# Performance work log

Measured on AMD Instinct MI355X. Metric: run time of the kernel, lower is better.

Reference implementation:

```python
import jax, jax.numpy as jnp
import numpy as np

N, E = 50000, 800000
IN, HID, H, OUT, NLAYERS = 128, 32, 4, 1, 3
F_HID = HID * H  # 128, width between layers


def _glorot(key, shape, scale=0.05):
    return jax.random.normal(key, shape, dtype=jnp.float32) * scale


def setup_inputs() -> dict:
    key = jax.random.key(0)
    ks = jax.random.split(key, 20)
    x = jax.random.normal(ks[0], (N, IN), dtype=jnp.float32)
    edge_index = jax.random.randint(ks[1], (2, E), 0, N, dtype=jnp.int64)
    # layer 0 params (in=IN)
    W_l0 = _glorot(ks[2], (IN, F_HID)); b_l0 = jnp.zeros((F_HID,), jnp.float32)
    W_r0 = _glorot(ks[3], (IN, F_HID)); b_r0 = jnp.zeros((F_HID,), jnp.float32)
    att0 = _glorot(ks[4], (H, HID));    bo0 = jnp.zeros((F_HID,), jnp.float32)
    # layers 1..NLAYERS-1 stacked (in=F_HID)
    L = NLAYERS - 1
    W_l = _glorot(ks[5], (L, F_HID, F_HID)); b_l = jnp.zeros((L, F_HID), jnp.float32)
    W_r = _glorot(ks[6], (L, F_HID, F_HID)); b_r = jnp.zeros((L, F_HID), jnp.float32)
    att = _glorot(ks[7], (L, H, HID));        bo = jnp.zeros((L, F_HID), jnp.float32)
    # final linear
    W_f = _glorot(ks[8], (F_HID, OUT)); b_f = jnp.zeros((OUT,), jnp.float32)
    return dict(x=x, edge_index=edge_index,
                W_l0=W_l0, b_l0=b_l0, W_r0=W_r0, b_r0=b_r0, att0=att0, bo0=bo0,
                W_l=W_l, b_l=b_l, W_r=W_r, b_r=b_r, att=att, bo=bo,
                W_f=W_f, b_f=b_f)


def gatv2_layer(x, src, dst, Wl, bl, Wr, br, a, bo):
    # x: [N, Fin] -> [N, H*HID]. PyG GATv2Conv, concat=True, slope=0.2.
    xl = (x @ Wl + bl).reshape(N, H, HID)  # source transform (messages)
    xr = (x @ Wr + br).reshape(N, H, HID)  # target transform
    z = jax.nn.leaky_relu(xl[src] + xr[dst], 0.2)        # [E', H, HID]
    logits = jnp.einsum('ehc,hc->eh', z, a)              # [E', H]
    m = jax.ops.segment_max(logits, dst, num_segments=N)
    m = jnp.where(jnp.isfinite(m), m, 0.0)
    ex = jnp.exp(logits - m[dst])
    denom = jax.ops.segment_sum(ex, dst, num_segments=N)
    alpha = ex / jnp.maximum(denom[dst], 1e-16)          # segment softmax per dst
    out = jax.ops.segment_sum(xl[src] * alpha[:, :, None], dst, num_segments=N)
    return out.reshape(N, F_HID) + bo


def reference(x, edge_index, W_l0, b_l0, W_r0, b_r0, att0, bo0,
              W_l, b_l, W_r, b_r, att, bo, W_f, b_f):
    loop = jnp.arange(N, dtype=edge_index.dtype)  # PyG default add_self_loops=True
    src = jnp.concatenate([edge_index[0], loop])
    dst = jnp.concatenate([edge_index[1], loop])
    # dropout is identity in eval mode
    h = jax.nn.elu(gatv2_layer(x, src, dst, W_l0, b_l0, W_r0, b_r0, att0, bo0))
    for i in range(NLAYERS - 1):
        h = jax.nn.elu(gatv2_layer(h, src, dst, W_l[i], b_l[i], W_r[i], b_r[i], att[i], bo[i]))
    return h @ W_f + b_f  # [N, OUT]
```

## Files before the change

kernel.cpp:

```cpp
#include <hip/hip_runtime.h>
#include <math.h>

#define N_NODES 50000
#define F 128
#define NEDGE 800000
#define NB_SCAN 49

static __device__ __forceinline__ int imin(int a, int b) { return a < b ? a : b; }

__global__ __launch_bounds__(256) void gemm128(
    const float* __restrict__ A,
    const float* __restrict__ Wl, const float* __restrict__ bl,
    const float* __restrict__ Wr, const float* __restrict__ br,
    float* __restrict__ xl, float* __restrict__ xr)
{
    const float* W = blockIdx.y ? Wr : Wl;
    const float* b = blockIdx.y ? br : bl;
    float*       O = blockIdx.y ? xr : xl;

    __shared__ float As[32][132];
    __shared__ float Ws[32][132];

    const int tid = threadIdx.x;
    const int tx = tid & 15, ty = tid >> 4;
    const int R0 = blockIdx.x * 128;

    float acc[8][8];
#pragma unroll
    for (int i = 0; i < 8; ++i)
#pragma unroll
        for (int j = 0; j < 8; ++j) acc[i][j] = 0.f;

    for (int kt = 0; kt < 4; ++kt) {
#pragma unroll
        for (int i = 0; i < 4; ++i) {
            int f = tid + i * 256;
            int row = f >> 3, kq = f & 7;
            int gr = R0 + row;
            float4 v = make_float4(0.f, 0.f, 0.f, 0.f);
            if (gr < N_NODES) v = *(const float4*)&A[(size_t)gr * F + kt * 32 + kq * 4];
            As[kq * 4 + 0][row] = v.x; As[kq * 4 + 1][row] = v.y;
            As[kq * 4 + 2][row] = v.z; As[kq * 4 + 3][row] = v.w;
        }
#pragma unroll
        for (int i = 0; i < 4; ++i) {
            int f = tid + i * 256;
            int k = f >> 5, cq = f & 31;
            *(float4*)&Ws[k][cq * 4] = *(const float4*)&W[(size_t)(kt * 32 + k) * F + cq * 4];
        }
        __syncthreads();
#pragma unroll
        for (int k = 0; k < 32; ++k) {
            float a[8], w[8];
            *(float4*)&a[0] = *(const float4*)&As[k][ty * 8];
            *(float4*)&a[4] = *(const float4*)&As[k][ty * 8 + 4];
            *(float4*)&w[0] = *(const float4*)&Ws[k][tx * 8];
            *(float4*)&w[4] = *(const float4*)&Ws[k][tx * 8 + 4];
#pragma unroll
            for (int i = 0; i < 8; ++i)
#pragma unroll
                for (int j = 0; j < 8; ++j) acc[i][j] += a[i] * w[j];
        }
        __syncthreads();
    }
#pragma unroll
    for (int i = 0; i < 8; ++i) {
        int gr = R0 + ty * 8 + i;
        if (gr < N_NODES) {
#pragma unroll
            for (int j = 0; j < 8; ++j) acc[i][j] += b[tx * 8 + j];
            *(float4*)&O[(size_t)gr * F + tx * 8]     = make_float4(acc[i][0], acc[i][1], acc[i][2], acc[i][3]);
            *(float4*)&O[(size_t)gr * F + tx * 8 + 4] = make_float4(acc[i][4], acc[i][5], acc[i][6], acc[i][7]);
        }
    }
}

__global__ void k_hist(const int* __restrict__ dst, int* __restrict__ deg)
{
    for (int i = blockIdx.x * blockDim.x + threadIdx.x; i < NEDGE;
         i += gridDim.x * blockDim.x)
        atomicAdd(&deg[dst[i]], 1);
}

__global__ __launch_bounds__(1024) void k_reduce(const int* __restrict__ deg, int* __restrict__ bsum)
{
    __shared__ int s[1024];
    int i = blockIdx.x * 1024 + threadIdx.x;
    s[threadIdx.x] = (i < N_NODES) ? deg[i] + 1 : 0;
    __syncthreads();
    for (int d = 512; d > 0; d >>= 1) {
        if (threadIdx.x < d) s[threadIdx.x] += s[threadIdx.x + d];
        __syncthreads();
    }
    if (threadIdx.x == 0) bsum[blockIdx.x] = s[0];
}

__global__ void k_scan_bsum(const int* __restrict__ bsum, int* __restrict__ boff, int nb)
{
    if (blockIdx.x == 0 && threadIdx.x == 0) {
        int run = 0;
        for (int bb = 0; bb < nb; ++bb) { boff[bb] = run; run += bsum[bb]; }
    }
}

__global__ __launch_bounds__(1024) void k_scan(const int* __restrict__ deg, const int* __restrict__ boff,
                                               int* __restrict__ off, int* __restrict__ cursor)
{
    __shared__ int s[1024];
    int i = blockIdx.x * 1024 + threadIdx.x;
    int v = (i < N_NODES) ? deg[i] + 1 : 0;
    s[threadIdx.x] = v;
    __syncthreads();
    for (int d = 1; d < 1024; d <<= 1) {
        int tv = (threadIdx.x >= d) ? s[threadIdx.x - d] : 0;
        __syncthreads();
        s[threadIdx.x] += tv;
        __syncthreads();
    }
    int excl = s[threadIdx.x] - v + boff[blockIdx.x];
    if (i < N_NODES) { off[i] = excl; cursor[i] = excl; }
    if (i == N_NODES - 1) off[N_NODES] = excl + v;
}

__global__ void k_scatter(const int* __restrict__ src, const int* __restrict__ dst,
                          int* __restrict__ cursor, int* __restrict__ adj)
{
    for (int i = blockIdx.x * blockDim.x + threadIdx.x; i < NEDGE;
         i += gridDim.x * blockDim.x) {
        int p = atomicAdd(&cursor[dst[i]], 1);
        adj[p] = src[i];
    }
}

__global__ void k_selfloop(int* __restrict__ cursor, int* __restrict__ adj)
{
    int i = blockIdx.x * blockDim.x + threadIdx.x;
    if (i < N_NODES) { int p = atomicAdd(&cursor[i], 1); adj[p] = i; }
}

__device__ __forceinline__ float edge_term(const float4 xlc, const float4 xrv,
                                           const float4 attv)
{
    float z0 = xlc.x + xrv.x, z1 = xlc.y + xrv.y;
    float z2 = xlc.z + xrv.z, z3 = xlc.w + xrv.w;
    z0 = fmaxf(z0, 0.f) + 0.2f * fminf(z0, 0.f);
    z1 = fmaxf(z1, 0.f) + 0.2f * fminf(z1, 0.f);
    z2 = fmaxf(z2, 0.f) + 0.2f * fminf(z2, 0.f);
    z3 = fmaxf(z3, 0.f) + 0.2f * fminf(z3, 0.f);
    float term = z0 * attv.x + z1 * attv.y + z2 * attv.z + z3 * attv.w;
    term += __shfl_xor(term, 4);
    term += __shfl_xor(term, 2);
    term += __shfl_xor(term, 1);
    return term;
}

template <int FUSE_FINAL>
__global__ __launch_bounds__(256) void gat_edge(
    const float* __restrict__ xl, const float* __restrict__ xr,
    const float* __restrict__ att, const float* __restrict__ bo,
    const int* __restrict__ off, const int* __restrict__ adj,
    float* __restrict__ out,
    const float* __restrict__ wf, const float* __restrict__ bf)
{
    const int node = blockIdx.x * 8 + (threadIdx.x >> 5);
    if (node >= N_NODES) return;
    const int t = threadIdx.x & 31;
    const float4* __restrict__ xl4 = (const float4*)xl;
    const float4 attv = ((const float4*)att)[t];
    const float4 xrv  = ((const float4*)xr)[(size_t)node * 32 + t];
    const int e0 = off[node], e1 = off[node + 1];
    const int deg = e1 - e0;
    const int nq = deg >> 2, rem = deg & 3;
    const int elast = e1 - 1;

    float m = -1e30f, ssum = 0.f;
    float4 acc = make_float4(0.f, 0.f, 0.f, 0.f);

    int base = e0;
    float4 buf0 = xl4[(size_t)adj[imin(base + 0, elast)] * 32 + t];
    float4 buf1 = xl4[(size_t)adj[imin(base + 1, elast)] * 32 + t];
    float4 buf2 = xl4[(size_t)adj[imin(base + 2, elast)] * 32 + t];
    float4 buf3 = xl4[(size_t)adj[imin(base + 3, elast)] * 32 + t];

    for (int q = 0; q < nq; ++q) {
        float4 x0 = buf0, x1 = buf1, x2 = buf2, x3 = buf3;
        base += 4;
        buf0 = xl4[(size_t)adj[imin(base + 0, elast)] * 32 + t];
        buf1 = xl4[(size_t)adj[imin(base + 1, elast)] * 32 + t];
        buf2 = xl4[(size_t)adj[imin(base + 2, elast)] * 32 + t];
        buf3 = xl4[(size_t)adj[imin(base + 3, elast)] * 32 + t];

        float t0 = edge_term(x0, xrv, attv);
        float t1 = edge_term(x1, xrv, attv);
        float t2 = edge_term(x2, xrv, attv);
        float t3 = edge_term(x3, xrv, attv);

        float qm = fmaxf(fmaxf(t0, t1), fmaxf(t2, t3));
        float nm = fmaxf(m, qm);
        float corr = __expf(m - nm);
        float p0 = __expf(t0 - nm);
        float p1 = __expf(t1 - nm);
        float p2 = __expf(t2 - nm);
        float p3 = __expf(t3 - nm);
        m = nm;
        ssum  = ssum  * corr + ((p0 + p1) + (p2 + p3));
        acc.x = acc.x * corr + (p0 * x0.x + p1 * x1.x + p2 * x2.x + p3 * x3.x);
        acc.y = acc.y * corr + (p0 * x0.y + p1 * x1.y + p2 * x2.y + p3 * x3.y);
        acc.z = acc.z * corr + (p0 * x0.z + p1 * x1.z + p2 * x2.z + p3 * x3.z);
        acc.w = acc.w * corr + (p0 * x0.w + p1 * x1.w + p2 * x2.w + p3 * x3.w);
    }

    if (rem > 0) {
        float tt = edge_term(buf0, xrv, attv);
        float d = tt - m, ev = __expf(-fabsf(d));
        float corr = (d > 0.f) ? ev : 1.f, p = (d > 0.f) ? 1.f : ev;
        m = fmaxf(m, tt);
        ssum  = ssum  * corr + p;
        acc.x = acc.x * corr + p * buf0.x;  acc.y = acc.y * corr + p * buf0.y;
        acc.z = acc.z * corr + p * buf0.z;  acc.w = acc.w * corr + p * buf0.w;
    }
    if (rem > 1) {
        float tt = edge_term(buf1, xrv, attv);
        float d = tt - m, ev = __expf(-fabsf(d));
        float corr = (d > 0.f) ? ev : 1.f, p = (d > 0.f) ? 1.f : ev;
        m = fmaxf(m, tt);
        ssum  = ssum  * corr + p;
        acc.x = acc.x * corr + p * buf1.x;  acc.y = acc.y * corr + p * buf1.y;
        acc.z = acc.z * corr + p * buf1.z;  acc.w = acc.w * corr + p * buf1.w;
    }
    if (rem > 2) {
        float tt = edge_term(buf2, xrv, attv);
        float d = tt - m, ev = __expf(-fabsf(d));
        float corr = (d > 0.f) ? ev : 1.f, p = (d > 0.f) ? 1.f : ev;
        m = fmaxf(m, tt);
        ssum  = ssum  * corr + p;
        acc.x = acc.x * corr + p * buf2.x;  acc.y = acc.y * corr + p * buf2.y;
        acc.z = acc.z * corr + p * buf2.z;  acc.w = acc.w * corr + p * buf2.w;
    }

    const float inv = 1.f / ssum;
    const float4 bov = ((const float4*)bo)[t];
    float4 o;
    o.x = acc.x * inv + bov.x;
    o.y = acc.y * inv + bov.y;
    o.z = acc.z * inv + bov.z;
    o.w = acc.w * inv + bov.w;
    o.x = (o.x > 0.f) ? o.x : expm1f(o.x);
    o.y = (o.y > 0.f) ? o.y : expm1f(o.y);
    o.z = (o.z > 0.f) ? o.z : expm1f(o.z);
    o.w = (o.w > 0.f) ? o.w : expm1f(o.w);

    if (FUSE_FINAL) {
        const float4 wfv = ((const float4*)wf)[t];
        float v = o.x * wfv.x + o.y * wfv.y + o.z * wfv.z + o.w * wfv.w;
        v += __shfl_xor(v, 16); v += __shfl_xor(v, 8); v += __shfl_xor(v, 4);
        v += __shfl_xor(v, 2);  v += __shfl_xor(v, 1);
        if (t == 0) out[node] = v + bf[0];
    } else {
        ((float4*)out)[(size_t)node * 32 + t] = o;
    }
}

extern "C" void kernel_launch(void* const* d_in, const int* in_sizes, int n_in,
                              void* d_out, int out_size, void* d_ws, size_t ws_size,
                              hipStream_t stream)
{
    const float* x    = (const float*)d_in[0];
    const int*   ei   = (const int*)  d_in[1];
    const float* W_l0 = (const float*)d_in[2];
    const float* b_l0 = (const float*)d_in[3];
    const float* W_r0 = (const float*)d_in[4];
    const float* b_r0 = (const float*)d_in[5];
    const float* att0 = (const float*)d_in[6];
    const float* bo0  = (const float*)d_in[7];
    const float* W_l  = (const float*)d_in[8];
    const float* b_l  = (const float*)d_in[9];
    const float* W_r  = (const float*)d_in[10];
    const float* b_r  = (const float*)d_in[11];
    const float* att  = (const float*)d_in[12];
    const float* bo   = (const float*)d_in[13];
    const float* W_f  = (const float*)d_in[14];
    const float* b_f  = (const float*)d_in[15];
    float* out = (float*)d_out;

    char* ws = (char*)d_ws;
    size_t o = 0;
    auto alloc = [&](size_t bytes) { void* p = ws + o; o += (bytes + 255) & ~(size_t)255; return p; };
    float* xl  = (float*)alloc((size_t)N_NODES * F * 4);
    float* xr  = (float*)alloc((size_t)N_NODES * F * 4);
    float* hb  = (float*)alloc((size_t)N_NODES * F * 4);
    int* deg   = (int*)alloc((size_t)N_NODES * 4);
    int* off   = (int*)alloc((size_t)(N_NODES + 1) * 4);
    int* cur   = (int*)alloc((size_t)N_NODES * 4);
    int* adj   = (int*)alloc((size_t)(NEDGE + N_NODES) * 4);
    int* bsum  = (int*)alloc(64 * 4);
    int* boff  = (int*)alloc(64 * 4);

    const int* srcv = ei;
    const int* dstv = ei + NEDGE;

    hipMemsetAsync(deg, 0, (size_t)N_NODES * 4, stream);
    k_hist<<<1024, 256, 0, stream>>>(dstv, deg);
    k_reduce<<<NB_SCAN, 1024, 0, stream>>>(deg, bsum);
    k_scan_bsum<<<1, 64, 0, stream>>>(bsum, boff, NB_SCAN);
    k_scan<<<NB_SCAN, 1024, 0, stream>>>(deg, boff, off, cur);
    k_scatter<<<1024, 256, 0, stream>>>(srcv, dstv, cur, adj);
    k_selfloop<<<(N_NODES + 255) / 256, 256, 0, stream>>>(cur, adj);

    const float* Ain = x;
    for (int l = 0; l < 3; ++l) {
        const float *Wlp, *blp, *Wrp, *brp, *attp, *bop;
        if (l == 0) {
            Wlp = W_l0; blp = b_l0; Wrp = W_r0; brp = b_r0; attp = att0; bop = bo0;
        } else {
            Wlp = W_l + (size_t)(l - 1) * F * F;
            blp = b_l + (size_t)(l - 1) * F;
            Wrp = W_r + (size_t)(l - 1) * F * F;
            brp = b_r + (size_t)(l - 1) * F;
            attp = att + (size_t)(l - 1) * F;
            bop = bo + (size_t)(l - 1) * F;
        }
        gemm128<<<dim3((N_NODES + 127) / 128, 2), 256, 0, stream>>>(
            Ain, Wlp, blp, Wrp, brp, xl, xr);
        if (l < 2) {
            gat_edge<0><<<(N_NODES + 7) / 8, 256, 0, stream>>>(
                xl, xr, attp, bop, off, adj, hb, W_f, b_f);
        } else {
            gat_edge<1><<<(N_NODES + 7) / 8, 256, 0, stream>>>(
                xl, xr, attp, bop, off, adj, out, W_f, b_f);
        }
        Ain = hb;
    }
}
```

Baseline: 551.1 us.

## Double-buffer GEMM shared tiles with register prefetch and halve row tile

Rewrites the dense transform GEMM to use double-buffered shared-memory tiles. The next K-slice is prefetched into registers while the current one is computed, and the row tile drops from 128 to 64 rows with a 4x8 per-thread micro-tile. Output columns are now split as two strided float4 groups. The goal is to hide global load latency and roughly double the block count for better occupancy on the many-CU GPU, at the cost of less register reuse per thread. The scatter kernel's grid is also resized to one thread per edge.

```diff
diff --git a/kernel.cpp b/kernel.cpp
--- a/kernel.cpp
+++ b/kernel.cpp
@@ -18,59 +18,102 @@
     const float* b = blockIdx.y ? br : bl;
     float*       O = blockIdx.y ? xr : xl;
 
-    __shared__ float As[32][132];
-    __shared__ float Ws[32][132];
+    __shared__ float As[2][32][68];
+    __shared__ float Ws[2][32][128];
 
     const int tid = threadIdx.x;
     const int tx = tid & 15, ty = tid >> 4;
-    const int R0 = blockIdx.x * 128;
-
-    float acc[8][8];
-#pragma unroll
-    for (int i = 0; i < 8; ++i)
+    const int R0 = blockIdx.x * 64;
+
+    const int arow = tid >> 3, akq = tid & 7;
+    const int wk = tid >> 5, wcq = tid & 31;
+
+    float acc[4][8];
+#pragma unroll
+    for (int i = 0; i < 4; ++i)
 #pragma unroll
         for (int j = 0; j < 8; ++j) acc[i][j] = 0.f;
 
+    float4 pa0, pa1, pw0, pw1, pw2, pw3;
+    {
+        int gr0 = R0 + arow, gr1 = R0 + arow + 32;
+        pa0 = (gr0 < N_NODES) ? *(const float4*)&A[(size_t)gr0 * F + akq * 4]
+                              : make_float4(0.f, 0.f, 0.f, 0.f);
+        pa1 = (gr1 < N_NODES) ? *(const float4*)&A[(size_t)gr1 * F + akq * 4]
+                              : make_float4(0.f, 0.f, 0.f, 0.f);
+        pw0 = *(const float4*)&W[(size_t)(wk +  0) * F + wcq * 4];
+        pw1 = *(const float4*)&W[(size_t)(wk +  8) * F + wcq * 4];
+        pw2 = *(const float4*)&W[(size_t)(wk + 16) * F + wcq * 4];
+        pw3 = *(const float4*)&W[(size_t)(wk + 24) * F + wcq * 4];
+    }
+    {
+        As[0][akq * 4 + 0][arow] = pa0.x; As[0][akq * 4 + 1][arow] = pa0.y;
+        As[0][akq * 4 + 2][arow] = pa0.z; As[0][akq * 4 + 3][arow] = pa0.w;
+        As[0][akq * 4 + 0][arow + 32] = pa1.x; As[0][akq * 4 + 1][arow + 32] = pa1.y;
+        As[0][akq * 4 + 2][arow + 32] = pa1.z; As[0][akq * 4 + 3][arow + 32] = pa1.w;
+        *(float4*)&Ws[0][wk +  0][wcq * 4] = pw0;
+        *(float4*)&Ws[0][wk +  8][wcq * 4] = pw1;
+        *(float4*)&Ws[0][wk + 16][wcq * 4] = pw2;
+        *(float4*)&Ws[0][wk + 24][wcq * 4] = pw3;
+    }
+    __syncthreads();
+
+    int cur = 0;
     for (int kt = 0; kt < 4; ++kt) {
-#pragma unroll
-        for (int i = 0; i < 4; ++i) {
-            int f = tid + i * 256;
-            int row = f >> 3, kq = f & 7;
-            int gr = R0 + row;
-            float4 v = make_float4(0.f, 0.f, 0.f, 0.f);
-            if (gr < N_NODES) v = *(const float4*)&A[(size_t)gr * F + kt * 32 + kq * 4];
-            As[kq * 4 + 0][row] = v.x; As[kq * 4 + 1][row] = v.y;
-            As[kq * 4 + 2][row] = v.z; As[kq * 4 + 3][row] = v.w;
-        }
-#pragma unroll
-        for (int i = 0; i < 4; ++i) {
-            int f = tid + i * 256;
-            int k = f >> 5, cq = f & 31;
-            *(float4*)&Ws[k][cq * 4] = *(const float4*)&W[(size_t)(kt * 32 + k) * F + cq * 4];
+        if (kt < 3) {
+            const int kb = (kt + 1) * 32;
+            int gr0 = R0 + arow, gr1 = R0 + arow + 32;
+            pa0 = (gr0 < N_NODES) ? *(const float4*)&A[(size_t)gr0 * F + kb + akq * 4]
+                                  : make_float4(0.f, 0.f, 0.f, 0.f);
+            pa1 = (gr1 < N_NODES) ? *(const float4*)&A[(size_t)gr1 * F + kb + akq * 4]
+                                  : make_float4(0.f, 0.f, 0.f, 0.f);
+            pw0 = *(const float4*)&W[(size_t)(kb + wk +  0) * F + wcq * 4];
+            pw1 = *(const float4*)&W[(size_t)(kb + wk +  8) * F + wcq * 4];
+            pw2 = *(const float4*)&W[(size_t)(kb + wk + 16) * F + wcq * 4];
+            pw3 = *(const float4*)&W[(size_t)(kb + wk + 24) * F + wcq * 4];
+        }
+#pragma unroll
+        for (int k = 0; k < 32; ++k) {
+            float4 a4 = *(const float4*)&As[cur][k][ty * 4];
+            float4 w0 = *(const float4*)&Ws[cur][k][tx * 4];
+            float4 w1 = *(const float4*)&Ws[cur][k][tx * 4 + 64];
+            float av[4] = {a4.x, a4.y, a4.z, a4.w};
+            float wv[8] = {w0.x, w0.y, w0.z, w0.w, w1.x, w1.y, w1.z, w1.w};
+#pragma unroll
+            for (int i = 0; i < 4; ++i)
+#pragma unroll
+                for (int j = 0; j < 8; ++j) acc[i][j] += av[i] * wv[j];
         }
         __syncthreads();
-#pragma unroll
-        for (int k = 0; k < 32; ++k) {
-            float a[8], w[8];
-            *(float4*)&a[0] = *(const float4*)&As[k][ty * 8];
-            *(float4*)&a[4] = *(const float4*)&As[k][ty * 8 + 4];
-            *(float4*)&w[0] = *(const float4*)&Ws[k][tx * 8];
-            *(float4*)&w[4] = *(const float4*)&Ws[k][tx * 8 + 4];
-#pragma unroll
-            for (int i = 0; i < 8; ++i)
-#pragma unroll
-                for (int j = 0; j < 8; ++j) acc[i][j] += a[i] * w[j];
-        }
-        __syncthreads();
-    }
-#pragma unroll
-    for (int i = 0; i < 8; ++i) {
-        int gr = R0 + ty * 8 + i;
+        if (kt < 3) {
+            int nxt = cur ^ 1;
+            As[nxt][akq * 4 + 0][arow] = pa0.x; As[nxt][akq * 4 + 1][arow] = pa0.y;
+            As[nxt][akq * 4 + 2][arow] = pa0.z; As[nxt][akq * 4 + 3][arow] = pa0.w;
+            As[nxt][akq * 4 + 0][arow + 32] = pa1.x; As[nxt][akq * 4 + 1][arow + 32] = pa1.y;
+            As[nxt][akq * 4 + 2][arow + 32] = pa1.z; As[nxt][akq * 4 + 3][arow + 32] = pa1.w;
+            *(float4*)&Ws[nxt][wk +  0][wcq * 4] = pw0;
+            *(float4*)&Ws[nxt][wk +  8][wcq * 4] = pw1;
+            *(float4*)&Ws[nxt][wk + 16][wcq * 4] = pw2;
+            *(float4*)&Ws[nxt][wk + 24][wcq * 4] = pw3;
+            __syncthreads();
+            cur = nxt;
+        }
+    }
+
+#pragma unroll
+    for (int i = 0; i < 4; ++i) {
+        int gr = R0 + ty * 4 + i;
         if (gr < N_NODES) {
-#pragma unroll
-            for (int j = 0; j < 8; ++j) acc[i][j] += b[tx * 8 + j];
-            *(float4*)&O[(size_t)gr * F + tx * 8]     = make_float4(acc[i][0], acc[i][1], acc[i][2], acc[i][3]);
-            *(float4*)&O[(size_t)gr * F + tx * 8 + 4] = make_float4(acc[i][4], acc[i][5], acc[i][6], acc[i][7]);
+            float4 o0 = make_float4(acc[i][0] + b[tx * 4 + 0],
+                                    acc[i][1] + b[tx * 4 + 1],
+                                    acc[i][2] + b[tx * 4 + 2],
+                                    acc[i][3] + b[tx * 4 + 3]);
+            float4 o1 = make_float4(acc[i][4] + b[tx * 4 + 64],
+                                    acc[i][5] + b[tx * 4 + 65],
+                                    acc[i][6] + b[tx * 4 + 66],
+                                    acc[i][7] + b[tx * 4 + 67]);
+            *(float4*)&O[(size_t)gr * F + tx * 4]      = o0;
+            *(float4*)&O[(size_t)gr * F + tx * 4 + 64] = o1;
         }
     }
 }
@@ -304,7 +347,7 @@
     k_reduce<<<NB_SCAN, 1024, 0, stream>>>(deg, bsum);
     k_scan_bsum<<<1, 64, 0, stream>>>(bsum, boff, NB_SCAN);
     k_scan<<<NB_SCAN, 1024, 0, stream>>>(deg, boff, off, cur);
-    k_scatter<<<1024, 256, 0, stream>>>(srcv, dstv, cur, adj);
+    k_scatter<<<(NEDGE + 255) / 256, 256, 0, stream>>>(srcv, dstv, cur, adj);
     k_selfloop<<<(N_NODES + 255) / 256, 256, 0, stream>>>(cur, adj);
 
     const float* Ain = x;
@@ -320,7 +363,7 @@
             attp = att + (size_t)(l - 1) * F;
             bop = bo + (size_t)(l - 1) * F;
         }
-        gemm128<<<dim3((N_NODES + 127) / 128, 2), 256, 0, stream>>>(
+        gemm128<<<dim3((N_NODES + 63) / 64, 2), 256, 0, stream>>>(
             Ain, Wlp, blp, Wrp, brp, xl, xr);
         if (l < 2) {
             gat_edge<0><<<(N_NODES + 7) / 8, 256, 0, stream>>>(
```

Result: slower. 656.1 us (+19.0%).
